# Kernel optimization log

Measured on AMD Instinct MI355X. Metric: run time of the kernel, lower is better.

Reference implementation:

```python
import jax, jax.numpy as jnp
import numpy as np


def setup_inputs() -> dict:
    key = jax.random.key(0)
    k1, k2, k3 = jax.random.split(key, 3)
    B, L, D, E = 32, 4096, 8, 64
    x = jax.random.normal(k1, (B, L, D), dtype=jnp.float32)
    W = jax.random.normal(k2, (D, E), dtype=jnp.float32)
    b = jax.random.normal(k3, (D, E), dtype=jnp.float32)
    return {"x": x, "W": W, "b": b}


def reference(x, W, b):
    # diag_embed(x) @ W + b  ==  x[..., None] * W + b  (elementwise broadcast)
    x_affine = x[..., None] * W + b            # [B, L, D, E]
    # split first embed channel (linear) from the rest (sin-activated)
    x0 = x_affine[..., :1]                     # [B, L, D, 1]
    xr = jnp.sin(x_affine[..., 1:])            # [B, L, D, E-1]
    out = jnp.concatenate([x0, xr], axis=-1)   # [B, L, D, E]
    B, L = x.shape[0], x.shape[1]
    return out.reshape(B, L, -1)               # [B, L, D*E]
```

## Files before the change

### kernel.cpp

```cpp
#include <hip/hip_runtime.h>
#include <math.h>


#define T2V_E   64
#define T2V_DE  512

__global__ __launch_bounds__(256) void t2v_kernel(
    const float* __restrict__ x,
    const float* __restrict__ W,
    const float* __restrict__ bias,
    float* __restrict__ out,
    int n4)
{
    __shared__ float4 sW[T2V_DE / 4];
    __shared__ float4 sB[T2V_DE / 4];
    const int t = threadIdx.x;
    if (t < T2V_DE / 4) {
        sW[t] = ((const float4*)W)[t];
        sB[t] = ((const float4*)bias)[t];
    }
    __syncthreads();

    const int stride = blockDim.x * gridDim.x;
    for (int i = blockIdx.x * blockDim.x + t; i < n4; i += stride) {
        const int i4 = i << 2;
        const float xv = x[i4 >> 6];
        const int wi = (i4 & (T2V_DE - 1)) >> 2;
        const float4 w = sW[wi];
        const float4 c = sB[wi];
        float4 a;
        a.x = fmaf(xv, w.x, c.x);
        a.y = fmaf(xv, w.y, c.y);
        a.z = fmaf(xv, w.z, c.z);
        a.w = fmaf(xv, w.w, c.w);
        float4 o;
        o.x = ((i4 & (T2V_E - 1)) == 0) ? a.x : __sinf(a.x);
        o.y = __sinf(a.y);
        o.z = __sinf(a.z);
        o.w = __sinf(a.w);
        ((float4*)out)[i] = o;
    }
}

extern "C" void kernel_launch(void* const* d_in, const int* in_sizes, int n_in,
                              void* d_out, int out_size, void* d_ws, size_t ws_size,
                              hipStream_t stream) {
    const float* x    = (const float*)d_in[0];
    const float* W    = (const float*)d_in[1];
    const float* bias = (const float*)d_in[2];
    float* out = (float*)d_out;

    const int n4 = out_size >> 2;
    const int threads = 256;
    const int blocks = 8192;
    t2v_kernel<<<blocks, threads, 0, stream>>>(x, W, bias, out, n4);
}
```

Before: 271.3 us.

## Use fixed-work blocks with nontemporal vector stores and hoisted weight loads

```diff
diff --git a/kernel.cpp b/kernel.cpp
--- a/kernel.cpp
+++ b/kernel.cpp
@@ -5,12 +5,13 @@
 #define T2V_E   64
 #define T2V_DE  512
 
+typedef float fx4 __attribute__((ext_vector_type(4)));
+
 __global__ __launch_bounds__(256) void t2v_kernel(
     const float* __restrict__ x,
     const float* __restrict__ W,
     const float* __restrict__ bias,
-    float* __restrict__ out,
-    int n4)
+    fx4* __restrict__ out)
 {
     __shared__ float4 sW[T2V_DE / 4];
     __shared__ float4 sB[T2V_DE / 4];
@@ -21,24 +22,26 @@
     }
     __syncthreads();
 
-    const int stride = blockDim.x * gridDim.x;
-    for (int i = blockIdx.x * blockDim.x + t; i < n4; i += stride) {
-        const int i4 = i << 2;
-        const float xv = x[i4 >> 6];
-        const int wi = (i4 & (T2V_DE - 1)) >> 2;
-        const float4 w = sW[wi];
-        const float4 c = sB[wi];
-        float4 a;
-        a.x = fmaf(xv, w.x, c.x);
-        a.y = fmaf(xv, w.y, c.y);
-        a.z = fmaf(xv, w.z, c.z);
-        a.w = fmaf(xv, w.w, c.w);
-        float4 o;
-        o.x = ((i4 & (T2V_E - 1)) == 0) ? a.x : __sinf(a.x);
-        o.y = __sinf(a.y);
-        o.z = __sinf(a.z);
-        o.w = __sinf(a.w);
-        ((float4*)out)[i] = o;
+    const int base = blockIdx.x * 1024 + t;
+
+    const int wi = (base & 127);
+    const float4 w = sW[wi];
+    const float4 c = sB[wi];
+
+#pragma unroll
+    for (int k = 0; k < 4; ++k) {
+        const int i = base + k * 256;
+        const float xv = x[i >> 4];
+        float ax = fmaf(xv, w.x, c.x);
+        float ay = fmaf(xv, w.y, c.y);
+        float az = fmaf(xv, w.z, c.z);
+        float aw = fmaf(xv, w.w, c.w);
+        fx4 o;
+        o.x = ((i & 15) == 0) ? ax : __sinf(ax);
+        o.y = __sinf(ay);
+        o.z = __sinf(az);
+        o.w = __sinf(aw);
+        __builtin_nontemporal_store(o, &out[i]);
     }
 }
 
@@ -48,10 +51,8 @@
     const float* x    = (const float*)d_in[0];
     const float* W    = (const float*)d_in[1];
     const float* bias = (const float*)d_in[2];
-    float* out = (float*)d_out;
+    fx4* out = (fx4*)d_out;
 
-    const int n4 = out_size >> 2;
-    const int threads = 256;
-    const int blocks = 8192;
-    t2v_kernel<<<blocks, threads, 0, stream>>>(x, W, bias, out, n4);
+    const int blocks = (out_size >> 2) / 1024;
+    t2v_kernel<<<blocks, 256, 0, stream>>>(x, W, bias, out);
 }
```

Measured after the change: 268.2 us. About the same (-1.1%).
